# Optimization experiments

Measured on AMD Instinct MI355X. Metric: run time of the kernel, lower is better.

## Reference

```python
import jax, jax.numpy as jnp
import numpy as np
from jax.ops import segment_sum, segment_max

N, E, G = 20000, 100000, 16
TILE, EMB, HID, OUT, FEAT, HEADS = 32, 128, 256, 512, 512, 8
SLOPE = 0.2


def setup_inputs() -> dict:
    key = jax.random.key(0)
    ks = jax.random.split(key, 20)
    def gn(k, shape, fan_in):
        return jax.random.normal(k, shape, jnp.float32) * (1.0 / np.sqrt(fan_in))
    return {
        "x": jax.random.normal(ks[0], (N, TILE), jnp.float32),
        "edge_index": jax.random.randint(ks[1], (2, E), 0, N, jnp.int32),
        "batch": jnp.sort(jax.random.randint(ks[2], (N,), 0, G, jnp.int32)),
        "W0": gn(ks[3], (TILE, EMB), TILE), "b0": jnp.zeros((EMB,), jnp.float32),
        "W1": gn(ks[4], (EMB, HEADS * HID), EMB),
        "a1s": gn(ks[5], (HEADS, HID), HID), "a1d": gn(ks[6], (HEADS, HID), HID),
        "b1": jnp.zeros((HEADS * HID,), jnp.float32),
        "W2": gn(ks[7], (HEADS * HID, HEADS * HID), HEADS * HID),
        "a2s": gn(ks[8], (HEADS, HID), HID), "a2d": gn(ks[9], (HEADS, HID), HID),
        "b2": jnp.zeros((HEADS * HID,), jnp.float32),
        "W3": gn(ks[10], (HEADS * HID, OUT), HEADS * HID),
        "a3s": gn(ks[11], (1, OUT), OUT), "a3d": gn(ks[12], (1, OUT), OUT),
        "b3": jnp.zeros((OUT,), jnp.float32),
        "Wf": gn(ks[13], (OUT, FEAT), OUT), "bf": jnp.zeros((FEAT,), jnp.float32),
    }


def gat_conv(x, src, dst, W, a_s, a_d, b, heads, ch, n):
    # PyG GATConv: linear, per-edge additive attention, segment softmax over dst, scatter-add
    h = (x @ W).reshape(n, heads, ch)                       # [N,H,C]
    e_src = jnp.einsum("nhc,hc->nh", h, a_s)                 # [N,H]
    e_dst = jnp.einsum("nhc,hc->nh", h, a_d)
    e = jax.nn.leaky_relu(e_src[src] + e_dst[dst], SLOPE)    # [E,H]
    m = segment_max(e, dst, num_segments=n)                  # [N,H]
    m = jax.lax.stop_gradient(jnp.where(jnp.isfinite(m), m, 0.0))
    ex = jnp.exp(e - m[dst])
    den = segment_sum(ex, dst, num_segments=n)
    alpha = ex / (den[dst] + 1e-16)                          # [E,H]
    out = segment_sum(h[src] * alpha[..., None], dst, num_segments=n)  # [N,H,C]
    return out.reshape(n, heads * ch) + b


def reference(x, edge_index, batch, W0, b0, W1, a1s, a1d, b1, W2, a2s, a2d, b2,
              W3, a3s, a3d, b3, Wf, bf):
    loop = jnp.arange(N, dtype=edge_index.dtype)             # PyG adds self-loops by default
    src = jnp.concatenate([edge_index[0], loop])
    dst = jnp.concatenate([edge_index[1], loop])
    h = jax.nn.leaky_relu(x @ W0 + b0, SLOPE)
    h = jax.nn.leaky_relu(gat_conv(h, src, dst, W1, a1s, a1d, b1, HEADS, HID, N), SLOPE)
    h = jax.nn.leaky_relu(gat_conv(h, src, dst, W2, a2s, a2d, b2, HEADS, HID, N), SLOPE)
    h = jax.nn.leaky_relu(gat_conv(h, src, dst, W3, a3s, a3d, b3, 1, OUT, N), SLOPE)
    sums = segment_sum(h, batch, num_segments=G)             # global_mean_pool
    cnt = segment_sum(jnp.ones((N,), h.dtype), batch, num_segments=G)
    mean = sums / jnp.maximum(cnt, 1.0)[:, None]
    return jax.nn.leaky_relu(mean @ Wf + bf, SLOPE)
```

## Files before the change

kernel.cpp:

```cpp
#include <hip/hip_runtime.h>
#include <hip/hip_bf16.h>

#define N_NODES 20000
#define N_EDGES 100000
#define ET (N_EDGES + N_NODES)
#define G_GRAPHS 16
#define SLOPE 0.2f

using short8  = __attribute__((ext_vector_type(8))) short;
using floatx4 = __attribute__((ext_vector_type(4))) float;

__device__ __forceinline__ float lrelu(float x) { return x > 0.f ? x : SLOPE * x; }

__device__ __forceinline__ float b2f(unsigned short u) {
    union { unsigned int i; float f; } v; v.i = ((unsigned int)u) << 16; return v.f;
}
__device__ __forceinline__ unsigned short f2b(float f) {
    union { float f; unsigned int i; } v; v.f = f;
    unsigned int i = v.i;
    return (unsigned short)((i + 0x7fffu + ((i >> 16) & 1u)) >> 16);
}

__device__ __forceinline__ void gld16(const void* g, void* l) {
    __builtin_amdgcn_global_load_lds((const __attribute__((address_space(1))) void*)g,
                                     (__attribute__((address_space(3))) void*)l, 16, 0, 0);
}

__device__ int dev_lower_bound(const int* a, int n, int key) {
    int lo = 0, hi = n;
    while (lo < hi) { int mid = (lo + hi) >> 1; if (a[mid] < key) lo = mid + 1; else hi = mid; }
    return lo;
}

__global__ void zero_kernel(int* __restrict__ p, int n) {
    int i = blockIdx.x * blockDim.x + threadIdx.x;
    if (i < n) p[i] = 0;
}

__global__ void count_kernel(const int* __restrict__ ei, int* __restrict__ counts) {
    int e = blockIdx.x * blockDim.x + threadIdx.x;
    if (e >= ET) return;
    int dst = (e < N_EDGES) ? ei[N_EDGES + e] : (e - N_EDGES);
    atomicAdd(&counts[dst], 1);
}

__global__ __launch_bounds__(1024) void scan_kernel(int* __restrict__ counts,
                                                    int* __restrict__ row_ptr) {
    __shared__ int sums[1024];
    int t = threadIdx.x;
    const int CH = (N_NODES + 1023) / 1024;
    int base = t * CH;
    int s = 0;
    for (int i = 0; i < CH; i++) { int idx = base + i; if (idx < N_NODES) s += counts[idx]; }
    sums[t] = s;
    __syncthreads();
    for (int off = 1; off < 1024; off <<= 1) {
        int v = (t >= off) ? sums[t - off] : 0;
        __syncthreads();
        sums[t] += v;
        __syncthreads();
    }
    int run = (t == 0) ? 0 : sums[t - 1];
    for (int i = 0; i < CH; i++) {
        int idx = base + i;
        if (idx < N_NODES) {
            int c = counts[idx];
            row_ptr[idx] = run;
            run += c;
            counts[idx] = 0;
        }
    }
    if (t == 1023) row_ptr[N_NODES] = run;
}

__global__ void fill_kernel(const int* __restrict__ ei, const int* __restrict__ row_ptr,
                            int* __restrict__ fill_cnt, int* __restrict__ col) {
    int e = blockIdx.x * blockDim.x + threadIdx.x;
    if (e >= ET) return;
    int src, dst;
    if (e < N_EDGES) { src = ei[e]; dst = ei[N_EDGES + e]; }
    else             { src = dst = e - N_EDGES; }
    int pos = atomicAdd(&fill_cnt[dst], 1);
    col[row_ptr[dst] + pos] = src;
}

__global__ void prep_kernel(const float* __restrict__ W1, const float* __restrict__ W2,
                            const float* __restrict__ W3, const float* __restrict__ a1s,
                            const float* __restrict__ a1d, unsigned short* __restrict__ W1t,
                            unsigned short* __restrict__ W2t, unsigned short* __restrict__ W3t,
                            float* __restrict__ w_es, float* __restrict__ w_ed) {
    int z = blockIdx.z;
    if (z == 3) {
        if (blockIdx.x >= 8 || blockIdx.y > 0 || threadIdx.x >= 128) return;
        int hd = blockIdx.x, k = threadIdx.x;
        const float* w   = W1 + (size_t)k * 2048 + hd * 256;
        const float* as_ = a1s + hd * 256;
        const float* ad_ = a1d + hd * 256;
        float s1 = 0.f, s2 = 0.f;
        for (int c = 0; c < 256; c++) { float wv = w[c]; s1 += wv * as_[c]; s2 += wv * ad_[c]; }
        w_es[k * 8 + hd] = s1;
        w_ed[k * 8 + hd] = s2;
        return;
    }
    const float* W; unsigned short* Wt; int K, N;
    if (z == 0)      { W = W1; Wt = W1t; K = 128;  N = 2048; }
    else if (z == 1) { W = W2; Wt = W2t; K = 2048; N = 2048; }
    else             { W = W3; Wt = W3t; K = 2048; N = 512;  }
    int bn = blockIdx.x * 32, bk = blockIdx.y * 32;
    if (bn >= N || bk >= K) return;
    __shared__ float tile[32][33];
    int tx = threadIdx.x & 31, ty = threadIdx.x >> 5;
#pragma unroll
    for (int p = 0; p < 32; p += 8)
        tile[ty + p][tx] = W[(size_t)(bk + ty + p) * N + bn + tx];
    __syncthreads();
#pragma unroll
    for (int p = 0; p < 32; p += 8)
        Wt[(size_t)(bn + ty + p) * K + bk + tx] = f2b(tile[tx][ty + p]);
}

__global__ void gemm0es_kernel(const float* __restrict__ x, const float* __restrict__ W0,
                               const float* __restrict__ b0, const float* __restrict__ w_es,
                               const float* __restrict__ w_ed, unsigned short* __restrict__ h0,
                               float* __restrict__ es, float* __restrict__ ed) {
    __shared__ float xr[32];
    __shared__ float red[2][16];
    int n = blockIdx.x, t = threadIdx.x;
    if (t < 32) xr[t] = x[n * 32 + t];
    __syncthreads();
    float acc = 0.f;
#pragma unroll
    for (int k = 0; k < 32; k++) acc += xr[k] * W0[k * 128 + t];
    float h = lrelu(acc + b0[t]);
    h0[(size_t)n * 128 + t] = f2b(h);
    float p[16];
#pragma unroll
    for (int hd = 0; hd < 8; hd++) {
        p[hd]     = h * w_es[t * 8 + hd];
        p[8 + hd] = h * w_ed[t * 8 + hd];
    }
#pragma unroll
    for (int m = 1; m < 64; m <<= 1)
#pragma unroll
        for (int i = 0; i < 16; i++) p[i] += __shfl_xor(p[i], m);
    int w = t >> 6, l = t & 63;
    if (l == 0)
#pragma unroll
        for (int i = 0; i < 16; i++) red[w][i] = p[i];
    __syncthreads();
    if (t < 8)       es[n * 8 + t] = red[0][t] + red[1][t];
    else if (t < 16) ed[n * 8 + (t - 8)] = red[0][t] + red[1][t];
}

__global__ __launch_bounds__(256) void agg1_wave(const unsigned short* __restrict__ h0,
                                                 const float* __restrict__ es,
                                                 const float* __restrict__ ed,
                                                 const int* __restrict__ row_ptr,
                                                 const int* __restrict__ col,
                                                 unsigned short* __restrict__ outp) {
    int wv = threadIdx.x >> 6, l = threadIdx.x & 63;
    int v = blockIdx.x * 4 + wv;
    if (v >= N_NODES) return;
    int rs = row_ptr[v], deg = row_ptr[v + 1] - rs;
    float edv[8], den[8], a0[8], a1[8];
#pragma unroll
    for (int hd = 0; hd < 8; hd++) { edv[hd] = ed[v * 8 + hd]; den[hd] = 0.f; a0[hd] = 0.f; a1[hd] = 0.f; }
    int sN = (deg > 0) ? col[rs] : 0;
    for (int e = 0; e < deg; e++) {
        int s = sN;
        if (e + 1 < deg) sN = col[rs + e + 1];
        unsigned int u = *(const unsigned int*)&h0[(size_t)s * 128 + l * 2];
        float x0 = b2f((unsigned short)(u & 0xffff)), x1 = b2f((unsigned short)(u >> 16));
#pragma unroll
        for (int hd = 0; hd < 8; hd++) {
            float a = __expf(lrelu(es[s * 8 + hd] + edv[hd]));
            den[hd] += a;
            a0[hd] += a * x0;
            a1[hd] += a * x1;
        }
    }
#pragma unroll
    for (int hd = 0; hd < 8; hd++) {
        float inv = 1.f / (den[hd] + 1e-16f);
        unsigned int o = (unsigned int)f2b(a0[hd] * inv) | ((unsigned int)f2b(a1[hd] * inv) << 16);
        *(unsigned int*)&outp[(size_t)v * 1024 + hd * 128 + l * 2] = o;
    }
}

__global__ __launch_bounds__(256) void gemm_mfma(const unsigned short* __restrict__ A,
                                                 const unsigned short* __restrict__ Bt,
                                                 unsigned short* __restrict__ C,
                                                 int M, int N, int K, int nx, int ny) {
    int lid = blockIdx.x;
    int k8 = lid & 7, jj = lid >> 3;
    int bx = jj % nx;
    int by = (jj / nx) * 8 + k8;
    if (by >= ny) return;
    __shared__ __align__(16) unsigned short As[128][64];
    __shared__ __align__(16) unsigned short Bs[128][64];
    int t = threadIdx.x;
    int w = t >> 6, l = t & 63;
    int r0 = by * 128, c0 = bx * 128;
    int wr = (w >> 1) * 64, wc = (w & 1) * 64;
    int srow = l >> 3;
    int gcb  = (l & 7) ^ srow;
    int m16 = l & 15, qb = l >> 4;
    floatx4 acc[4][4] = {};

    for (int k0 = 0; k0 < K; k0 += 64) {
        __syncthreads();
#pragma unroll
        for (int q = 0; q < 4; q++) {
            int row = w * 32 + q * 8 + srow;
            int ga = min(r0 + row, M - 1);
            gld16(A + (size_t)ga * K + k0 + gcb * 8, &As[w * 32 + q * 8][0]);
            gld16(Bt + (size_t)(c0 + row) * K + k0 + gcb * 8, &Bs[w * 32 + q * 8][0]);
        }
        __syncthreads();
#pragma unroll
        for (int kh = 0; kh < 2; kh++) {
            int roff = (((kh * 4 + qb) ^ (m16 & 7)) * 8);
            short8 af[4], bfr[4];
#pragma unroll
            for (int i = 0; i < 4; i++) af[i] = *(const short8*)&As[wr + i * 16 + m16][roff];
#pragma unroll
            for (int j = 0; j < 4; j++) bfr[j] = *(const short8*)&Bs[wc + j * 16 + m16][roff];
#pragma unroll
            for (int i = 0; i < 4; i++)
#pragma unroll
                for (int j = 0; j < 4; j++)
                    acc[i][j] = __builtin_amdgcn_mfma_f32_16x16x32_bf16(bfr[j], af[i], acc[i][j], 0, 0, 0);
        }
    }
    int quad = l >> 4;
#pragma unroll
    for (int i = 0; i < 4; i++) {
        int r = r0 + wr + i * 16 + m16;
        if (r < M) {
#pragma unroll
            for (int j = 0; j < 4; j++) {
                int c = c0 + wc + j * 16 + quad * 4;
                ushort4 o = make_ushort4(f2b(acc[i][j][0]), f2b(acc[i][j][1]),
                                         f2b(acc[i][j][2]), f2b(acc[i][j][3]));
                *(ushort4*)&C[(size_t)r * N + c] = o;
            }
        }
    }
}

__global__ __launch_bounds__(256) void gemm_mfma_h1(const unsigned short* __restrict__ A,
                                                    const unsigned short* __restrict__ Bt,
                                                    const float* __restrict__ bias,
                                                    unsigned short* __restrict__ C,
                                                    int M) {
    const int N = 2048, K = 128;
    __shared__ __align__(16) unsigned short As[128][64];
    __shared__ __align__(16) unsigned short Bs[128][64];
    int t = threadIdx.x;
    int w = t >> 6, l = t & 63;
    int r0 = blockIdx.y * 128, c0 = blockIdx.x * 128;
    int wr = (w >> 1) * 64, wc = (w & 1) * 64;
    int srow = l >> 3;
    int gcb  = (l & 7) ^ srow;
    int m16 = l & 15, qb = l >> 4;
    int aoff = (c0 >> 8) * 128;
    floatx4 acc[4][4] = {};

    for (int k0 = 0; k0 < K; k0 += 64) {
        __syncthreads();
#pragma unroll
        for (int q = 0; q < 4; q++) {
            int row = w * 32 + q * 8 + srow;
            int ga = min(r0 + row, M - 1);
            gld16(A + (size_t)ga * 1024 + aoff + k0 + gcb * 8, &As[w * 32 + q * 8][0]);
            gld16(Bt + (size_t)(c0 + row) * K + k0 + gcb * 8, &Bs[w * 32 + q * 8][0]);
        }
        __syncthreads();
#pragma unroll
        for (int kh = 0; kh < 2; kh++) {
            int roff = (((kh * 4 + qb) ^ (m16 & 7)) * 8);
            short8 af[4], bfr[4];
#pragma unroll
            for (int i = 0; i < 4; i++) af[i] = *(const short8*)&As[wr + i * 16 + m16][roff];
#pragma unroll
            for (int j = 0; j < 4; j++) bfr[j] = *(const short8*)&Bs[wc + j * 16 + m16][roff];
#pragma unroll
            for (int i = 0; i < 4; i++)
#pragma unroll
                for (int j = 0; j < 4; j++)
                    acc[i][j] = __builtin_amdgcn_mfma_f32_16x16x32_bf16(bfr[j], af[i], acc[i][j], 0, 0, 0);
        }
    }
    int quad = l >> 4;
#pragma unroll
    for (int i = 0; i < 4; i++) {
        int r = r0 + wr + i * 16 + m16;
        if (r < M) {
#pragma unroll
            for (int j = 0; j < 4; j++) {
                int c = c0 + wc + j * 16 + quad * 4;
                ushort4 o = make_ushort4(f2b(lrelu(acc[i][j][0] + bias[c + 0])),
                                         f2b(lrelu(acc[i][j][1] + bias[c + 1])),
                                         f2b(lrelu(acc[i][j][2] + bias[c + 2])),
                                         f2b(lrelu(acc[i][j][3] + bias[c + 3])));
                *(ushort4*)&C[(size_t)r * N + c] = o;
            }
        }
    }
}

__global__ void att8_kernel(const unsigned short* __restrict__ h, const float* __restrict__ a_s,
                            const float* __restrict__ a_d, float* __restrict__ es,
                            float* __restrict__ ed) {
    int n = blockIdx.x, t = threadIdx.x;
    int hd = t >> 5, l = t & 31;
    const unsigned short* hr = h + (size_t)n * 2048 + hd * 256 + l * 8;
    const float* as_ = a_s + hd * 256 + l * 8;
    const float* ad_ = a_d + hd * 256 + l * 8;
    uint4 u = *(const uint4*)hr;
    float v[8] = { b2f((unsigned short)(u.x & 0xffff)), b2f((unsigned short)(u.x >> 16)),
                   b2f((unsigned short)(u.y & 0xffff)), b2f((unsigned short)(u.y >> 16)),
                   b2f((unsigned short)(u.z & 0xffff)), b2f((unsigned short)(u.z >> 16)),
                   b2f((unsigned short)(u.w & 0xffff)), b2f((unsigned short)(u.w >> 16)) };
    float s1 = 0.f, s2 = 0.f;
#pragma unroll
    for (int j = 0; j < 8; j++) { s1 += v[j] * as_[j]; s2 += v[j] * ad_[j]; }
    for (int m = 16; m >= 1; m >>= 1) { s1 += __shfl_xor(s1, m); s2 += __shfl_xor(s2, m); }
    if (l == 0) { es[n * 8 + hd] = s1; ed[n * 8 + hd] = s2; }
}

__global__ void att1_kernel(const unsigned short* __restrict__ h, const float* __restrict__ a_s,
                            const float* __restrict__ a_d, float* __restrict__ es,
                            float* __restrict__ ed) {
    int n = blockIdx.x, l = threadIdx.x;
    const unsigned short* hr = h + (size_t)n * 512 + l * 8;
    const float* as_ = a_s + l * 8;
    const float* ad_ = a_d + l * 8;
    uint4 u = *(const uint4*)hr;
    float v[8] = { b2f((unsigned short)(u.x & 0xffff)), b2f((unsigned short)(u.x >> 16)),
                   b2f((unsigned short)(u.y & 0xffff)), b2f((unsigned short)(u.y >> 16)),
                   b2f((unsigned short)(u.z & 0xffff)), b2f((unsigned short)(u.z >> 16)),
                   b2f((unsigned short)(u.w & 0xffff)), b2f((unsigned short)(u.w >> 16)) };
    float s1 = 0.f, s2 = 0.f;
#pragma unroll
    for (int j = 0; j < 8; j++) { s1 += v[j] * as_[j]; s2 += v[j] * ad_[j]; }
    for (int m = 32; m >= 1; m >>= 1) { s1 += __shfl_xor(s1, m); s2 += __shfl_xor(s2, m); }
    if (l == 0) { es[n] = s1; ed[n] = s2; }
}

template <int H, int C>
__global__ __launch_bounds__(256) void agg_wave(const unsigned short* __restrict__ hmid,
                                                const float* __restrict__ es,
                                                const float* __restrict__ ed,
                                                const int* __restrict__ row_ptr,
                                                const int* __restrict__ col,
                                                const float* __restrict__ bias,
                                                unsigned short* __restrict__ out) {
    constexpr int HC = H * C;
    constexpr int CH = HC / 512;
    int wv = threadIdx.x >> 6, l = threadIdx.x & 63;
    int v = blockIdx.x * 4 + wv;
    if (v >= N_NODES) return;
    int rs = row_ptr[v], deg = row_ptr[v + 1] - rs;
    int hd[CH];
    float edv[CH], den[CH], acc[CH][8];
#pragma unroll
    for (int c = 0; c < CH; c++) {
        hd[c] = (c * 512 + l * 8) / C;
        edv[c] = ed[v * H + hd[c]];
        den[c] = 0.f;
#pragma unroll
        for (int k = 0; k < 8; k++) acc[c][k] = 0.f;
    }
    int e = 0;
    for (; e + 2 <= deg; e += 2) {
        int s0 = col[rs + e], s1 = col[rs + e + 1];
        const unsigned short* hr0 = hmid + (size_t)s0 * HC + l * 8;
        const unsigned short* hr1 = hmid + (size_t)s1 * HC + l * 8;
        uint4 u0[CH], u1[CH];
#pragma unroll
        for (int c = 0; c < CH; c++) { u0[c] = *(const uint4*)(hr0 + c * 512); u1[c] = *(const uint4*)(hr1 + c * 512); }
        float ex0[CH], ex1[CH];
#pragma unroll
        for (int c = 0; c < CH; c++) {
            ex0[c] = __expf(lrelu(es[s0 * H + hd[c]] + edv[c]));
            ex1[c] = __expf(lrelu(es[s1 * H + hd[c]] + edv[c]));
            den[c] += ex0[c] + ex1[c];
        }
#pragma unroll
        for (int c = 0; c < CH; c++) {
            float a = ex0[c], b = ex1[c];
            acc[c][0] += a * b2f((unsigned short)(u0[c].x & 0xffff)) + b * b2f((unsigned short)(u1[c].x & 0xffff));
            acc[c][1] += a * b2f((unsigned short)(u0[c].x >> 16))    + b * b2f((unsigned short)(u1[c].x >> 16));
            acc[c][2] += a * b2f((unsigned short)(u0[c].y & 0xffff)) + b * b2f((unsigned short)(u1[c].y & 0xffff));
            acc[c][3] += a * b2f((unsigned short)(u0[c].y >> 16))    + b * b2f((unsigned short)(u1[c].y >> 16));
            acc[c][4] += a * b2f((unsigned short)(u0[c].z & 0xffff)) + b * b2f((unsigned short)(u1[c].z & 0xffff));
            acc[c][5] += a * b2f((unsigned short)(u0[c].z >> 16))    + b * b2f((unsigned short)(u1[c].z >> 16));
            acc[c][6] += a * b2f((unsigned short)(u0[c].w & 0xffff)) + b * b2f((unsigned short)(u1[c].w & 0xffff));
            acc[c][7] += a * b2f((unsigned short)(u0[c].w >> 16))    + b * b2f((unsigned short)(u1[c].w >> 16));
        }
    }
    if (e < deg) {
        int s = col[rs + e];
        const unsigned short* hr = hmid + (size_t)s * HC + l * 8;
#pragma unroll
        for (int c = 0; c < CH; c++) {
            uint4 u = *(const uint4*)(hr + c * 512);
            float a = __expf(lrelu(es[s * H + hd[c]] + edv[c]));
            den[c] += a;
            acc[c][0] += a * b2f((unsigned short)(u.x & 0xffff));
            acc[c][1] += a * b2f((unsigned short)(u.x >> 16));
            acc[c][2] += a * b2f((unsigned short)(u.y & 0xffff));
            acc[c][3] += a * b2f((unsigned short)(u.y >> 16));
            acc[c][4] += a * b2f((unsigned short)(u.z & 0xffff));
            acc[c][5] += a * b2f((unsigned short)(u.z >> 16));
            acc[c][6] += a * b2f((unsigned short)(u.w & 0xffff));
            acc[c][7] += a * b2f((unsigned short)(u.w >> 16));
        }
    }
#pragma unroll
    for (int c = 0; c < CH; c++) {
        float inv = 1.f / (den[c] + 1e-16f);
        unsigned short o[8];
#pragma unroll
        for (int k = 0; k < 8; k++)
            o[k] = f2b(lrelu(acc[c][k] * inv + bias[c * 512 + l * 8 + k]));
        *(uint4*)&out[(size_t)v * HC + c * 512 + l * 8] = *(const uint4*)o;
    }
}

__global__ void pool_kernel(const unsigned short* __restrict__ h3, const int* __restrict__ batch,
                            float* __restrict__ msum) {
    int b0 = blockIdx.x * 128, t = threadIdx.x;
    int nend = min(b0 + 128, N_NODES);
    int curg = batch[b0];
    float s0 = 0.f, s1 = 0.f;
    for (int n = b0; n < nend; n++) {
        int g = batch[n];
        if (g != curg) {
            atomicAdd(&msum[curg * 512 + t * 2], s0);
            atomicAdd(&msum[curg * 512 + t * 2 + 1], s1);
            s0 = s1 = 0.f; curg = g;
        }
        unsigned int u = *(const unsigned int*)&h3[(size_t)n * 512 + t * 2];
        s0 += b2f((unsigned short)(u & 0xffff));
        s1 += b2f((unsigned short)(u >> 16));
    }
    atomicAdd(&msum[curg * 512 + t * 2], s0);
    atomicAdd(&msum[curg * 512 + t * 2 + 1], s1);
}

__global__ void final_kernel(const float* __restrict__ msum, const int* __restrict__ batch,
                             const float* __restrict__ Wf, const float* __restrict__ bf,
                             float* __restrict__ out) {
    int g = blockIdx.x, t = threadIdx.x;
    __shared__ float mr[512];
    __shared__ float sinv;
    if (t == 0) {
        int st = dev_lower_bound(batch, N_NODES, g);
        int en = dev_lower_bound(batch, N_NODES, g + 1);
        sinv = 1.f / fmaxf((float)(en - st), 1.f);
    }
    __syncthreads();
    for (int c = t; c < 512; c += 256) mr[c] = msum[g * 512 + c] * sinv;
    __syncthreads();
    for (int j = t; j < 512; j += 256) {
        float s = 0.f;
        for (int k = 0; k < 512; k++) s += mr[k] * Wf[k * 512 + j];
        out[g * 512 + j] = lrelu(s + bf[j]);
    }
}

extern "C" void kernel_launch(void* const* d_in, const int* in_sizes, int n_in,
                              void* d_out, int out_size, void* d_ws, size_t ws_size,
                              hipStream_t stream) {
    const float* x   = (const float*)d_in[0];
    const int*   ei  = (const int*)d_in[1];
    const int*   bat = (const int*)d_in[2];
    const float* W0  = (const float*)d_in[3];
    const float* b0  = (const float*)d_in[4];
    const float* W1  = (const float*)d_in[5];
    const float* a1s = (const float*)d_in[6];
    const float* a1d = (const float*)d_in[7];
    const float* b1  = (const float*)d_in[8];
    const float* W2  = (const float*)d_in[9];
    const float* a2s = (const float*)d_in[10];
    const float* a2d = (const float*)d_in[11];
    const float* b2  = (const float*)d_in[12];
    const float* W3  = (const float*)d_in[13];
    const float* a3s = (const float*)d_in[14];
    const float* a3d = (const float*)d_in[15];
    const float* b3  = (const float*)d_in[16];
    const float* Wf  = (const float*)d_in[17];
    const float* bf  = (const float*)d_in[18];
    float* out = (float*)d_out;

    char* p = (char*)d_ws;
    unsigned short* bufA = (unsigned short*)p; p += (size_t)N_NODES * 2048 * 2;
    unsigned short* bufB = (unsigned short*)p; p += (size_t)N_NODES * 2048 * 2;
    unsigned short* h0   = (unsigned short*)p; p += (size_t)N_NODES * 128 * 2;
    unsigned short* W1t  = (unsigned short*)p; p += (size_t)2048 * 128 * 2;
    unsigned short* W2t  = (unsigned short*)p; p += (size_t)2048 * 2048 * 2;
    unsigned short* W3t  = (unsigned short*)p; p += (size_t)512 * 2048 * 2;
    float* es   = (float*)p; p += (size_t)N_NODES * 8 * 4;
    float* ed   = (float*)p; p += (size_t)N_NODES * 8 * 4;
    float* w_es = (float*)p; p += 128 * 8 * 4;
    float* w_ed = (float*)p; p += 128 * 8 * 4;
    int* counts  = (int*)p; p += (size_t)N_NODES * 4;
    float* msum  = (float*)p; p += 16 * 512 * 4;
    int* row_ptr = (int*)p; p += (size_t)(N_NODES + 1) * 4;
    int* col     = (int*)p; p += (size_t)ET * 4;
    const int ZN = N_NODES + 16 * 512;

    zero_kernel<<<(ZN + 255) / 256, 256, 0, stream>>>(counts, ZN);
    count_kernel<<<(ET + 255) / 256, 256, 0, stream>>>(ei, counts);
    scan_kernel<<<1, 1024, 0, stream>>>(counts, row_ptr);
    fill_kernel<<<(ET + 255) / 256, 256, 0, stream>>>(ei, row_ptr, counts, col);

    prep_kernel<<<dim3(64, 64, 4), 256, 0, stream>>>(W1, W2, W3, a1s, a1d,
                                                     W1t, W2t, W3t, w_es, w_ed);

    gemm0es_kernel<<<N_NODES, 128, 0, stream>>>(x, W0, b0, w_es, w_ed, h0, es, ed);

    const int NY = (N_NODES + 127) / 128;
    const int NYP = ((NY + 7) / 8) * 8;
    dim3 g12(2048 / 128, NY);
    int g2 = 16 * NYP;
    int g3 = 4 * NYP;
    int aggb = (N_NODES + 3) / 4;

    agg1_wave<<<aggb, 256, 0, stream>>>(h0, es, ed, row_ptr, col, bufB);
    gemm_mfma_h1<<<g12, 256, 0, stream>>>(bufB, W1t, b1, bufA, N_NODES);

    gemm_mfma<<<g2, 256, 0, stream>>>(bufA, W2t, bufB, N_NODES, 2048, 2048, 16, NY);
    att8_kernel<<<N_NODES, 256, 0, stream>>>(bufB, a2s, a2d, es, ed);
    agg_wave<8, 256><<<aggb, 256, 0, stream>>>(bufB, es, ed, row_ptr, col, b2, bufA);

    gemm_mfma<<<g3, 256, 0, stream>>>(bufA, W3t, bufB, N_NODES, 512, 2048, 4, NY);
    att1_kernel<<<N_NODES, 64, 0, stream>>>(bufB, a3s, a3d, es, ed);
    agg_wave<1, 512><<<aggb, 256, 0, stream>>>(bufB, es, ed, row_ptr, col, b3, bufA);

    pool_kernel<<<(N_NODES + 127) / 128, 256, 0, stream>>>(bufA, bat, msum);
    final_kernel<<<G_GRAPHS, 256, 0, stream>>>(msum, bat, Wf, bf, out);
}
```

Baseline: 733.2 us.

## Fold layer-3 attention projections into W3 and compute scores in layer-2 aggregation

Precomputes W3·a3s and W3·a3d in the prep kernel, then computes the layer-3 source and destination attention scores inside the layer-2 aggregation epilogue from the bf16 outputs. This removes the separate att1 kernel launch and its re-read of the layer-3 GEMM output. It also unrolls the layer-1 aggregation edge loop by two to overlap gathers. Scores now come from bf16 inputs dotted with fp32-folded weights rather than from the bf16 GEMM output, which changes rounding slightly.

```diff
diff --git a/kernel.cpp b/kernel.cpp
--- a/kernel.cpp
+++ b/kernel.cpp
@@ -86,9 +86,11 @@
 
 __global__ void prep_kernel(const float* __restrict__ W1, const float* __restrict__ W2,
                             const float* __restrict__ W3, const float* __restrict__ a1s,
-                            const float* __restrict__ a1d, unsigned short* __restrict__ W1t,
+                            const float* __restrict__ a1d, const float* __restrict__ a3s,
+                            const float* __restrict__ a3d, unsigned short* __restrict__ W1t,
                             unsigned short* __restrict__ W2t, unsigned short* __restrict__ W3t,
-                            float* __restrict__ w_es, float* __restrict__ w_ed) {
+                            float* __restrict__ w_es, float* __restrict__ w_ed,
+                            float* __restrict__ w3es, float* __restrict__ w3ed) {
     int z = blockIdx.z;
     if (z == 3) {
         if (blockIdx.x >= 8 || blockIdx.y > 0 || threadIdx.x >= 128) return;
@@ -102,6 +104,16 @@
         w_ed[k * 8 + hd] = s2;
         return;
     }
+    if (z == 4) {
+        if (blockIdx.x >= 8 || blockIdx.y > 0) return;
+        int k = blockIdx.x * 256 + threadIdx.x;
+        const float* w = W3 + (size_t)k * 512;
+        float s1 = 0.f, s2 = 0.f;
+        for (int c = 0; c < 512; c++) { float wv = w[c]; s1 += wv * a3s[c]; s2 += wv * a3d[c]; }
+        w3es[k] = s1;
+        w3ed[k] = s2;
+        return;
+    }
     const float* W; unsigned short* Wt; int K, N;
     if (z == 0)      { W = W1; Wt = W1t; K = 128;  N = 2048; }
     else if (z == 1) { W = W2; Wt = W2t; K = 2048; N = 2048; }
@@ -165,10 +177,24 @@
     float edv[8], den[8], a0[8], a1[8];
 #pragma unroll
     for (int hd = 0; hd < 8; hd++) { edv[hd] = ed[v * 8 + hd]; den[hd] = 0.f; a0[hd] = 0.f; a1[hd] = 0.f; }
-    int sN = (deg > 0) ? col[rs] : 0;
-    for (int e = 0; e < deg; e++) {
-        int s = sN;
-        if (e + 1 < deg) sN = col[rs + e + 1];
+    int e = 0;
+    for (; e + 2 <= deg; e += 2) {
+        int s0 = col[rs + e], s1 = col[rs + e + 1];
+        unsigned int u0 = *(const unsigned int*)&h0[(size_t)s0 * 128 + l * 2];
+        unsigned int u1 = *(const unsigned int*)&h0[(size_t)s1 * 128 + l * 2];
+        float x00 = b2f((unsigned short)(u0 & 0xffff)), x01 = b2f((unsigned short)(u0 >> 16));
+        float x10 = b2f((unsigned short)(u1 & 0xffff)), x11 = b2f((unsigned short)(u1 >> 16));
+#pragma unroll
+        for (int hd = 0; hd < 8; hd++) {
+            float aa = __expf(lrelu(es[s0 * 8 + hd] + edv[hd]));
+            float bb = __expf(lrelu(es[s1 * 8 + hd] + edv[hd]));
+            den[hd] += aa + bb;
+            a0[hd] += aa * x00 + bb * x10;
+            a1[hd] += aa * x01 + bb * x11;
+        }
+    }
+    if (e < deg) {
+        int s = col[rs + e];
         unsigned int u = *(const unsigned int*)&h0[(size_t)s * 128 + l * 2];
         float x0 = b2f((unsigned short)(u & 0xffff)), x1 = b2f((unsigned short)(u >> 16));
 #pragma unroll
@@ -329,33 +355,18 @@
     if (l == 0) { es[n * 8 + hd] = s1; ed[n * 8 + hd] = s2; }
 }
 
-__global__ void att1_kernel(const unsigned short* __restrict__ h, const float* __restrict__ a_s,
-                            const float* __restrict__ a_d, float* __restrict__ es,
-                            float* __restrict__ ed) {
-    int n = blockIdx.x, l = threadIdx.x;
-    const unsigned short* hr = h + (size_t)n * 512 + l * 8;
-    const float* as_ = a_s + l * 8;
-    const float* ad_ = a_d + l * 8;
-    uint4 u = *(const uint4*)hr;
-    float v[8] = { b2f((unsigned short)(u.x & 0xffff)), b2f((unsigned short)(u.x >> 16)),
-                   b2f((unsigned short)(u.y & 0xffff)), b2f((unsigned short)(u.y >> 16)),
-                   b2f((unsigned short)(u.z & 0xffff)), b2f((unsigned short)(u.z >> 16)),
-                   b2f((unsigned short)(u.w & 0xffff)), b2f((unsigned short)(u.w >> 16)) };
-    float s1 = 0.f, s2 = 0.f;
-#pragma unroll
-    for (int j = 0; j < 8; j++) { s1 += v[j] * as_[j]; s2 += v[j] * ad_[j]; }
-    for (int m = 32; m >= 1; m >>= 1) { s1 += __shfl_xor(s1, m); s2 += __shfl_xor(s2, m); }
-    if (l == 0) { es[n] = s1; ed[n] = s2; }
-}
-
-template <int H, int C>
+template <int H, int C, bool FOLD>
 __global__ __launch_bounds__(256) void agg_wave(const unsigned short* __restrict__ hmid,
                                                 const float* __restrict__ es,
                                                 const float* __restrict__ ed,
                                                 const int* __restrict__ row_ptr,
                                                 const int* __restrict__ col,
                                                 const float* __restrict__ bias,
-                                                unsigned short* __restrict__ out) {
+                                                unsigned short* __restrict__ out,
+                                                const float* __restrict__ w3es,
+                                                const float* __restrict__ w3ed,
+                                                float* __restrict__ es3,
+                                                float* __restrict__ ed3) {
     constexpr int HC = H * C;
     constexpr int CH = HC / 512;
     int wv = threadIdx.x >> 6, l = threadIdx.x & 63;
@@ -418,14 +429,27 @@
             acc[c][7] += a * b2f((unsigned short)(u.w >> 16));
         }
     }
+    float s1 = 0.f, s2 = 0.f;
 #pragma unroll
     for (int c = 0; c < CH; c++) {
         float inv = 1.f / (den[c] + 1e-16f);
         unsigned short o[8];
 #pragma unroll
-        for (int k = 0; k < 8; k++)
-            o[k] = f2b(lrelu(acc[c][k] * inv + bias[c * 512 + l * 8 + k]));
+        for (int k = 0; k < 8; k++) {
+            float fv = lrelu(acc[c][k] * inv + bias[c * 512 + l * 8 + k]);
+            o[k] = f2b(fv);
+            if constexpr (FOLD) {
+                float hv = b2f(o[k]);
+                s1 += hv * w3es[c * 512 + l * 8 + k];
+                s2 += hv * w3ed[c * 512 + l * 8 + k];
+            }
+        }
         *(uint4*)&out[(size_t)v * HC + c * 512 + l * 8] = *(const uint4*)o;
+    }
+    if constexpr (FOLD) {
+#pragma unroll
+        for (int m = 1; m < 64; m <<= 1) { s1 += __shfl_xor(s1, m); s2 += __shfl_xor(s2, m); }
+        if (l == 0) { es3[v] = s1; ed3[v] = s2; }
     }
 }
 
@@ -504,8 +528,12 @@
     unsigned short* W3t  = (unsigned short*)p; p += (size_t)512 * 2048 * 2;
     float* es   = (float*)p; p += (size_t)N_NODES * 8 * 4;
     float* ed   = (float*)p; p += (size_t)N_NODES * 8 * 4;
+    float* es3  = (float*)p; p += (size_t)N_NODES * 4;
+    float* ed3  = (float*)p; p += (size_t)N_NODES * 4;
     float* w_es = (float*)p; p += 128 * 8 * 4;
     float* w_ed = (float*)p; p += 128 * 8 * 4;
+    float* w3es = (float*)p; p += 2048 * 4;
+    float* w3ed = (float*)p; p += 2048 * 4;
     int* counts  = (int*)p; p += (size_t)N_NODES * 4;
     float* msum  = (float*)p; p += 16 * 512 * 4;
     int* row_ptr = (int*)p; p += (size_t)(N_NODES + 1) * 4;
@@ -517,8 +545,8 @@
     scan_kernel<<<1, 1024, 0, stream>>>(counts, row_ptr);
     fill_kernel<<<(ET + 255) / 256, 256, 0, stream>>>(ei, row_ptr, counts, col);
 
-    prep_kernel<<<dim3(64, 64, 4), 256, 0, stream>>>(W1, W2, W3, a1s, a1d,
-                                                     W1t, W2t, W3t, w_es, w_ed);
+    prep_kernel<<<dim3(64, 64, 5), 256, 0, stream>>>(W1, W2, W3, a1s, a1d, a3s, a3d,
+                                                     W1t, W2t, W3t, w_es, w_ed, w3es, w3ed);
 
     gemm0es_kernel<<<N_NODES, 128, 0, stream>>>(x, W0, b0, w_es, w_ed, h0, es, ed);
 
@@ -534,11 +562,12 @@
 
     gemm_mfma<<<g2, 256, 0, stream>>>(bufA, W2t, bufB, N_NODES, 2048, 2048, 16, NY);
     att8_kernel<<<N_NODES, 256, 0, stream>>>(bufB, a2s, a2d, es, ed);
-    agg_wave<8, 256><<<aggb, 256, 0, stream>>>(bufB, es, ed, row_ptr, col, b2, bufA);
+    agg_wave<8, 256, true><<<aggb, 256, 0, stream>>>(bufB, es, ed, row_ptr, col, b2, bufA,
+                                                     w3es, w3ed, es3, ed3);
 
     gemm_mfma<<<g3, 256, 0, stream>>>(bufA, W3t, bufB, N_NODES, 512, 2048, 4, NY);
-    att1_kernel<<<N_NODES, 64, 0, stream>>>(bufB, a3s, a3d, es, ed);
-    agg_wave<1, 512><<<aggb, 256, 0, stream>>>(bufB, es, ed, row_ptr, col, b3, bufA);
+    agg_wave<1, 512, false><<<aggb, 256, 0, stream>>>(bufB, es3, ed3, row_ptr, col, b3, bufA,
+                                                      nullptr, nullptr, nullptr, nullptr);
 
     pool_kernel<<<(N_NODES + 127) / 128, 256, 0, stream>>>(bufA, bat, msum);
     final_kernel<<<G_GRAPHS, 256, 0, stream>>>(msum, bat, Wf, bf, out);
```

Result: slower. 763.4 us (+4.1%).
